# Kernel optimization log

Measured on AMD Instinct MI355X. Metric: run time of the kernel, lower is better.

The kernel has to match this reference:

```python
import jax, jax.numpy as jnp
import numpy as np

HIDDEN = 768
HEADS = 12
HEAD_DIM = HIDDEN // HEADS
NORM = float(np.sqrt(HIDDEN))  # module divides by sqrt(hidden_size), not sqrt(head_dim)


def setup_inputs() -> dict:
    key = jax.random.key(0)
    ks = jax.random.split(key, 7)
    B, S, H = 8, 1024, HIDDEN
    scale = 0.02
    return {
        "hidden_states": jax.random.normal(ks[0], (B, S, H), dtype=jnp.float32),
        "Wq": jax.random.normal(ks[1], (H, H), dtype=jnp.float32) * scale,
        "bq": jax.random.normal(ks[2], (H,), dtype=jnp.float32) * scale,
        "Wk": jax.random.normal(ks[3], (H, H), dtype=jnp.float32) * scale,
        "bk": jax.random.normal(ks[4], (H,), dtype=jnp.float32) * scale,
        "Wv": jax.random.normal(ks[5], (H, H), dtype=jnp.float32) * scale,
        "bv": jax.random.normal(ks[6], (H,), dtype=jnp.float32) * scale,
    }


def reference(hidden_states, Wq, bq, Wk, bk, Wv, bv):
    B, S, H = hidden_states.shape
    def heads(x):  # [B,S,H] -> [B,nh,S,hd]
        return x.reshape(B, S, HEADS, HEAD_DIM).transpose(0, 2, 1, 3)
    q = heads(hidden_states @ Wq + bq)
    k = heads(hidden_states @ Wk + bk)
    v = heads(hidden_states @ Wv + bv)
    # naive quadratic attention (world_size=1 ring): scores materialized
    scores = jnp.einsum("bhqd,bhkd->bhqk", q, k) / NORM
    probs = jax.nn.softmax(scores, axis=-1)  # dropout prob = 0.0
    ctx = jnp.einsum("bhqk,bhkd->bhqd", probs, v)
    # [B,nh,S,hd] -> [B,S,H]
    return ctx.transpose(0, 2, 1, 3).reshape(B, S, H)
```

## Files before the change

### kernel.cpp

```cpp
#include <hip/hip_runtime.h>
#include <hip/hip_bf16.h>
#include <stdint.h>

typedef __attribute__((ext_vector_type(8))) short short8;
typedef __attribute__((ext_vector_type(4))) float f32x4;
typedef __attribute__((ext_vector_type(4))) int i32x4;
typedef __attribute__((ext_vector_type(2))) int i32x2;
typedef __attribute__((ext_vector_type(4))) unsigned short u16x4;

#define HIDDEN 768
#define HEADS 12
#define HD 64
#define NB 8
#define SEQ 1024
#define MTOT (NB*SEQ)
#define QSCALE 0.05205887314427834f

typedef const __attribute__((address_space(1))) uint32_t* gas1_t;
typedef __attribute__((address_space(3))) uint32_t* las3_t;
#define GL_LDS16(g, l) __builtin_amdgcn_global_load_lds((gas1_t)(g), (las3_t)(l), 16, 0, 0)

static __device__ __forceinline__ unsigned short f2bf(float f){
  uint32_t u = __builtin_bit_cast(uint32_t, f);
  u += 0x7fffu + ((u >> 16) & 1u);
  return (unsigned short)(u >> 16);
}
static __device__ __forceinline__ float fexp2(float x){
#if __has_builtin(__builtin_amdgcn_exp2f)
  return __builtin_amdgcn_exp2f(x);
#else
  return exp2f(x);
#endif
}

__global__ void convert_x_kernel(const float* __restrict__ x, unsigned short* __restrict__ xb){
  int i = blockIdx.x * 256 + threadIdx.x;
  float4 v = reinterpret_cast<const float4*>(x)[i];
  u16x4 o;
  o[0]=f2bf(v.x); o[1]=f2bf(v.y); o[2]=f2bf(v.z); o[3]=f2bf(v.w);
  reinterpret_cast<u16x4*>(xb)[i] = o;
}

__global__ void transpose_w_kernel(const float* __restrict__ Wq, const float* __restrict__ Wk,
                                   const float* __restrict__ Wv, unsigned short* __restrict__ Wt){
  __shared__ float t[32][33];
  int z = blockIdx.z;
  const float* W = (z==0) ? Wq : ((z==1) ? Wk : Wv);
  unsigned short* o = Wt + (size_t)z * HIDDEN * HIDDEN;
  int n0 = blockIdx.x * 32, k0 = blockIdx.y * 32;
  int x = threadIdx.x & 31, y0 = threadIdx.x >> 5;
#pragma unroll
  for(int p=0;p<4;p++){ int y = y0 + p*8; t[y][x] = W[(size_t)(k0+y)*HIDDEN + n0 + x]; }
  __syncthreads();
#pragma unroll
  for(int p=0;p<4;p++){ int y = y0 + p*8; o[(size_t)(n0+y)*HIDDEN + k0 + x] = f2bf(t[x][y]); }
}

__global__ __launch_bounds__(256, 4) void gemm_qkv_kernel(
    const unsigned short* __restrict__ Xb, const unsigned short* __restrict__ Wt,
    const float* __restrict__ bq, const float* __restrict__ bk, const float* __restrict__ bv,
    unsigned short* __restrict__ Qg, unsigned short* __restrict__ Kg, unsigned short* __restrict__ Vt)
{
  __shared__ alignas(16) unsigned short lA[64*64];
  __shared__ alignas(16) unsigned short lB[128*64];
  int wgid = blockIdx.x;
  int xcd = wgid & 7, idx = wgid >> 3;
  int y = xcd + 8*(idx/18);
  int within = idx % 18;
  int xb = within % 6, z = within / 6;
  const unsigned short* W = Wt + (size_t)z*HIDDEN*HIDDEN;
  const float* bias = (z==0) ? bq : ((z==1) ? bk : bv);
  int m0 = y * 64, n0 = xb * 128;
  int tid = threadIdx.x;
  int w = tid >> 6, lane = tid & 63, l16 = lane & 15, g = lane >> 4;
  int wm = w >> 1, wn = w & 1;
  f32x4 acc[2][4] = {};
  for(int kt=0; kt<HIDDEN; kt+=64){
    __syncthreads();
#pragma unroll
    for(int p=0;p<2;p++){
      int t2 = p*256 + tid;
      int r = t2 >> 3;
      int cb = (((t2 & 7) << 4) ^ ((r & 7) << 4));
      GL_LDS16(Xb + (size_t)(m0 + r)*HIDDEN + kt + (cb >> 1), lA + p*2048 + w*512);
    }
#pragma unroll
    for(int p=0;p<4;p++){
      int t2 = p*256 + tid;
      int r = t2 >> 3;
      int cb = (((t2 & 7) << 4) ^ ((r & 7) << 4));
      GL_LDS16(W + (size_t)(n0 + r)*HIDDEN + kt + (cb >> 1), lB + p*2048 + w*512);
    }
    __syncthreads();
#pragma unroll
    for(int kk=0;kk<2;kk++){
      short8 af[2], bf[4];
#pragma unroll
      for(int i=0;i<2;i++){
        int row = wm*32 + i*16 + l16;
        af[i] = *reinterpret_cast<const short8*>(
            reinterpret_cast<const unsigned char*>(lA) + row*128 + ((kk*64 + g*16) ^ ((row&7)<<4)));
      }
#pragma unroll
      for(int j=0;j<4;j++){
        int row = wn*64 + j*16 + l16;
        bf[j] = *reinterpret_cast<const short8*>(
            reinterpret_cast<const unsigned char*>(lB) + row*128 + ((kk*64 + g*16) ^ ((row&7)<<4)));
      }
#pragma unroll
      for(int i=0;i<2;i++)
#pragma unroll
        for(int j=0;j<4;j++)
          acc[i][j] = __builtin_amdgcn_mfma_f32_16x16x32_bf16(af[i], bf[j], acc[i][j], 0, 0, 0);
    }
  }
  if(z == 2){
#pragma unroll
    for(int i=0;i<2;i++){
      int mb = m0 + wm*32 + i*16 + g*4;
      int b = mb >> 10, s = mb & 1023;
#pragma unroll
      for(int j=0;j<4;j++){
        int n = n0 + wn*64 + j*16 + l16;
        float bi = bias[n];
        int h = n >> 6, d = n & 63;
        u16x4 pk;
#pragma unroll
        for(int r=0;r<4;r++) pk[r] = f2bf(acc[i][j][r] + bi);
        *reinterpret_cast<u16x4*>(Vt + ((size_t)(b*HEADS + h)*HD + d)*SEQ + s) = pk;
      }
    }
  } else {
    unsigned short* out = (z==0) ? Qg : Kg;
#pragma unroll
    for(int i=0;i<2;i++){
      int mb = m0 + wm*32 + i*16 + g*4;
#pragma unroll
      for(int j=0;j<4;j++){
        int n = n0 + wn*64 + j*16 + l16;
        float bi = bias[n];
        int h = n >> 6, d = n & 63;
#pragma unroll
        for(int r=0;r<4;r++){
          int m = mb + r;
          int b = m >> 10, s = m & 1023;
          float cv = acc[i][j][r] + bi;
          if(z == 0) cv *= QSCALE;
          out[((size_t)(b*HEADS + h)*SEQ + s)*HD + d] = f2bf(cv);
        }
      }
    }
  }
}

__global__ __launch_bounds__(256, 3) void attn_kernel(
    const unsigned short* __restrict__ Qg, const unsigned short* __restrict__ Kg,
    const unsigned short* __restrict__ Vt, float* __restrict__ out)
{
  __shared__ alignas(16) unsigned short lK[2][64*64];
  __shared__ alignas(16) unsigned short lV[2][64*64];
  int wgid = blockIdx.x;
  int xcd = wgid & 7, ix = wgid >> 3;
  int bh = xcd*12 + (ix >> 3), qb = ix & 7;
  int b = bh / HEADS, h = bh % HEADS;
  int tid = threadIdx.x, w = tid >> 6, lane = tid & 63, l16 = lane & 15, g = lane >> 4;

  const unsigned short* Qbase = Qg + ((size_t)bh*SEQ + qb*128 + w*32)*HD;
  short8 qA0 = *reinterpret_cast<const short8*>(Qbase + l16*HD + g*8);
  short8 qA1 = *reinterpret_cast<const short8*>(Qbase + l16*HD + 32 + g*8);
  short8 qB0 = *reinterpret_cast<const short8*>(Qbase + (16+l16)*HD + g*8);
  short8 qB1 = *reinterpret_cast<const short8*>(Qbase + (16+l16)*HD + 32 + g*8);

  f32x4 oacc[2][4] = {};
  float lpart[2] = {0.f, 0.f};

  int sw = (l16 & 7) << 4;
  int ro0 = l16*128 + ((g*16) ^ sw);
  int ro1 = l16*128 + ((64 + g*16) ^ sw);
  int vo00 = l16*128 + ((      8*g) ^ sw);
  int vo01 = l16*128 + ((32  + 8*g) ^ sw);
  int vo10 = l16*128 + ((64  + 8*g) ^ sw);
  int vo11 = l16*128 + ((96  + 8*g) ^ sw);
  const unsigned char* lKb = reinterpret_cast<const unsigned char*>(&lK[0][0]);
  const unsigned char* lVb = reinterpret_cast<const unsigned char*>(&lV[0][0]);

  int r0 = tid >> 3;
  int cb0 = (((tid & 7) << 4) ^ ((r0 & 7) << 4)) >> 1;
  const unsigned short* gK0 = Kg + (size_t)bh*SEQ*HD + r0*HD + cb0;
  const unsigned short* gV0 = Vt + (size_t)bh*HD*SEQ + r0*SEQ + cb0;

#define STAGE(B, t) do { \
    GL_LDS16(gK0 + (t)*4096,          &lK[B][0] + w*512); \
    GL_LDS16(gK0 + (t)*4096 + 2048,   &lK[B][0] + 2048 + w*512); \
    GL_LDS16(gV0 + (t)*64,            &lV[B][0] + w*512); \
    GL_LDS16(gV0 + (t)*64 + 32*SEQ,   &lV[B][0] + 2048 + w*512); \
  } while(0)

#define SMPV(SREG, LP, OA) do { \
    int Wlo[4], Whi[4]; \
    _Pragma("unroll") for(int j=0;j<4;j++){ \
      float p0=fexp2(SREG[j][0]), p1=fexp2(SREG[j][1]); \
      float p2=fexp2(SREG[j][2]), p3=fexp2(SREG[j][3]); \
      LP += (p0+p1)+(p2+p3); \
      asm("v_cvt_pk_bf16_f32 %0, %1, %2" : "=v"(Wlo[j]) : "v"(p0), "v"(p1)); \
      asm("v_cvt_pk_bf16_f32 %0, %1, %2" : "=v"(Whi[j]) : "v"(p2), "v"(p3)); } \
    _Pragma("unroll") for(int m=0;m<2;m++){ \
      i32x4 cc; cc[0]=Wlo[2*m]; cc[1]=Whi[2*m]; cc[2]=Wlo[2*m+1]; cc[3]=Whi[2*m+1]; \
      short8 pB = __builtin_bit_cast(short8, cc); \
      _Pragma("unroll") for(int jn=0;jn<4;jn++) \
        OA[jn] = __builtin_amdgcn_mfma_f32_16x16x32_bf16(vf[jn][m], pB, OA[jn], 0,0,0); } \
  } while(0)

#define TILE(CUR, kt, HAS_NEXT) do { \
    if(HAS_NEXT) STAGE((CUR)^1, (kt)+1); \
    short8 kf[4][2]; \
    _Pragma("unroll") for(int j=0;j<4;j++){ \
      kf[j][0] = *reinterpret_cast<const short8*>(lKb + (CUR)*8192 + j*2048 + ro0); \
      kf[j][1] = *reinterpret_cast<const short8*>(lKb + (CUR)*8192 + j*2048 + ro1); } \
    short8 vf[4][2]; \
    _Pragma("unroll") for(int jn=0;jn<4;jn++){ \
      { i32x2 vl = *reinterpret_cast<const i32x2*>(lVb + (CUR)*8192 + jn*2048 + vo00); \
        i32x2 vh = *reinterpret_cast<const i32x2*>(lVb + (CUR)*8192 + jn*2048 + vo01); \
        i32x4 vc; vc[0]=vl[0]; vc[1]=vl[1]; vc[2]=vh[0]; vc[3]=vh[1]; \
        vf[jn][0] = __builtin_bit_cast(short8, vc); } \
      { i32x2 vl = *reinterpret_cast<const i32x2*>(lVb + (CUR)*8192 + jn*2048 + vo10); \
        i32x2 vh = *reinterpret_cast<const i32x2*>(lVb + (CUR)*8192 + jn*2048 + vo11); \
        i32x4 vc; vc[0]=vl[0]; vc[1]=vl[1]; vc[2]=vh[0]; vc[3]=vh[1]; \
        vf[jn][1] = __builtin_bit_cast(short8, vc); } } \
    f32x4 s0[4], s1[4]; \
    _Pragma("unroll") for(int j=0;j<4;j++){ \
      f32x4 zz = {}; \
      zz    = __builtin_amdgcn_mfma_f32_16x16x32_bf16(kf[j][0], qA0, zz, 0,0,0); \
      s0[j] = __builtin_amdgcn_mfma_f32_16x16x32_bf16(kf[j][1], qA1, zz, 0,0,0); } \
    _Pragma("unroll") for(int j=0;j<4;j++){ \
      f32x4 zz = {}; \
      zz    = __builtin_amdgcn_mfma_f32_16x16x32_bf16(kf[j][0], qB0, zz, 0,0,0); \
      s1[j] = __builtin_amdgcn_mfma_f32_16x16x32_bf16(kf[j][1], qB1, zz, 0,0,0); } \
    SMPV(s0, lpart[0], oacc[0]); \
    SMPV(s1, lpart[1], oacc[1]); \
    __syncthreads(); \
  } while(0)

  STAGE(0, 0);
  __syncthreads();

  for(int kt=0; kt<SEQ/64; kt+=2){
    TILE(0, kt, true);
    TILE(1, kt+1, (kt+1) < SEQ/64 - 1);
  }

#pragma unroll
  for(int rg=0;rg<2;rg++){
    float tot = lpart[rg];
    tot += __shfl_xor(tot, 16, 64);
    tot += __shfl_xor(tot, 32, 64);
    float invl = 1.0f / tot;
    int s = qb*128 + w*32 + rg*16 + l16;
    float* orow = out + ((size_t)b*SEQ + s)*HIDDEN + h*HD + 4*g;
#pragma unroll
    for(int jn=0;jn<4;jn++){
      float4 val;
      val.x = oacc[rg][jn][0]*invl; val.y = oacc[rg][jn][1]*invl;
      val.z = oacc[rg][jn][2]*invl; val.w = oacc[rg][jn][3]*invl;
      *reinterpret_cast<float4*>(orow + 16*jn) = val;
    }
  }
#undef STAGE
#undef SMPV
#undef TILE
}

extern "C" void kernel_launch(void* const* d_in, const int* in_sizes, int n_in,
                              void* d_out, int out_size, void* d_ws, size_t ws_size,
                              hipStream_t stream) {
  const float* hs = (const float*)d_in[0];
  const float* Wq = (const float*)d_in[1];
  const float* bq = (const float*)d_in[2];
  const float* Wk = (const float*)d_in[3];
  const float* bk = (const float*)d_in[4];
  const float* Wv = (const float*)d_in[5];
  const float* bv = (const float*)d_in[6];
  float* out = (float*)d_out;

  char* ws = (char*)d_ws;
  unsigned short* Xb = (unsigned short*)ws;
  unsigned short* Wt = (unsigned short*)(ws + (size_t)12582912);
  unsigned short* Qg = (unsigned short*)(ws + (size_t)16121856);
  unsigned short* Kg = Qg + (size_t)MTOT*HIDDEN;
  unsigned short* Vt = Kg + (size_t)MTOT*HIDDEN;

  convert_x_kernel<<<MTOT*HIDDEN/4/256, 256, 0, stream>>>(hs, Xb);
  transpose_w_kernel<<<dim3(24,24,3), 256, 0, stream>>>(Wq, Wk, Wv, Wt);
  gemm_qkv_kernel<<<2304, 256, 0, stream>>>(Xb, Wt, bq, bk, bv, Qg, Kg, Vt);
  attn_kernel<<<768, 256, 0, stream>>>(Qg, Kg, Vt, out);
}
```

Measured before the change: 90.48 us.

## Double-buffer LDS tiles in QKV GEMM to overlap loads with MFMA

The QKV projection GEMM now uses two LDS buffers for the A and B tiles. It issues the global-to-LDS loads for the next k-tile before computing on the current one, and needs one barrier per iteration instead of two. Global address arithmetic is also hoisted out of the loop. This is meant to hide global load latency behind MFMA work, at the cost of twice the LDS per block (48KB), which may limit occupancy to fewer than the 4 blocks the launch bounds request.

```diff
diff --git a/kernel.cpp b/kernel.cpp
--- a/kernel.cpp
+++ b/kernel.cpp
@@ -61,8 +61,8 @@
     const float* __restrict__ bq, const float* __restrict__ bk, const float* __restrict__ bv,
     unsigned short* __restrict__ Qg, unsigned short* __restrict__ Kg, unsigned short* __restrict__ Vt)
 {
-  __shared__ alignas(16) unsigned short lA[64*64];
-  __shared__ alignas(16) unsigned short lB[128*64];
+  __shared__ alignas(16) unsigned short lA[2][64*64];
+  __shared__ alignas(16) unsigned short lB[2][128*64];
   int wgid = blockIdx.x;
   int xcd = wgid & 7, idx = wgid >> 3;
   int y = xcd + 8*(idx/18);
@@ -74,46 +74,47 @@
   int tid = threadIdx.x;
   int w = tid >> 6, lane = tid & 63, l16 = lane & 15, g = lane >> 4;
   int wm = w >> 1, wn = w & 1;
+
+  int rs = tid >> 3;
+  int cbs = (((tid & 7) << 4) ^ ((rs & 7) << 4)) >> 1;
+  const unsigned short* gA0 = Xb + (size_t)(m0 + rs)*HIDDEN + cbs;
+  const unsigned short* gB0 = W  + (size_t)(n0 + rs)*HIDDEN + cbs;
+  const unsigned char* lAb = reinterpret_cast<const unsigned char*>(&lA[0][0]);
+  const unsigned char* lBb = reinterpret_cast<const unsigned char*>(&lB[0][0]);
+
   f32x4 acc[2][4] = {};
-  for(int kt=0; kt<HIDDEN; kt+=64){
+
+#define STAGE(BF, t) do { \
+    GL_LDS16(gA0 + (t)*64,                    &lA[BF][0] + w*512); \
+    GL_LDS16(gA0 + (size_t)32*HIDDEN + (t)*64, &lA[BF][0] + 2048 + w*512); \
+    _Pragma("unroll") for(int p=0;p<4;p++) \
+      GL_LDS16(gB0 + (size_t)p*32*HIDDEN + (t)*64, &lB[BF][0] + p*2048 + w*512); \
+  } while(0)
+
+#define COMPUTE(CUR) do { _Pragma("unroll") for(int kk=0;kk<2;kk++){ \
+    short8 af[2], bf[4]; \
+    _Pragma("unroll") for(int i=0;i<2;i++){ \
+      int row = wm*32 + i*16 + l16; \
+      af[i] = *reinterpret_cast<const short8*>( \
+          lAb + (CUR)*8192 + row*128 + ((kk*64 + g*16) ^ ((row&7)<<4))); } \
+    _Pragma("unroll") for(int j=0;j<4;j++){ \
+      int row = wn*64 + j*16 + l16; \
+      bf[j] = *reinterpret_cast<const short8*>( \
+          lBb + (CUR)*16384 + row*128 + ((kk*64 + g*16) ^ ((row&7)<<4))); } \
+    _Pragma("unroll") for(int i=0;i<2;i++) \
+      _Pragma("unroll") for(int j=0;j<4;j++) \
+        acc[i][j] = __builtin_amdgcn_mfma_f32_16x16x32_bf16(af[i], bf[j], acc[i][j], 0, 0, 0); \
+  } } while(0)
+
+  STAGE(0, 0);
+  __syncthreads();
+  for(int t=0; t<12; t++){
+    int cur = t & 1;
+    if(t < 11) STAGE(cur^1, t+1);
+    COMPUTE(cur);
     __syncthreads();
-#pragma unroll
-    for(int p=0;p<2;p++){
-      int t2 = p*256 + tid;
-      int r = t2 >> 3;
-      int cb = (((t2 & 7) << 4) ^ ((r & 7) << 4));
-      GL_LDS16(Xb + (size_t)(m0 + r)*HIDDEN + kt + (cb >> 1), lA + p*2048 + w*512);
-    }
-#pragma unroll
-    for(int p=0;p<4;p++){
-      int t2 = p*256 + tid;
-      int r = t2 >> 3;
-      int cb = (((t2 & 7) << 4) ^ ((r & 7) << 4));
-      GL_LDS16(W + (size_t)(n0 + r)*HIDDEN + kt + (cb >> 1), lB + p*2048 + w*512);
-    }
-    __syncthreads();
-#pragma unroll
-    for(int kk=0;kk<2;kk++){
-      short8 af[2], bf[4];
-#pragma unroll
-      for(int i=0;i<2;i++){
-        int row = wm*32 + i*16 + l16;
-        af[i] = *reinterpret_cast<const short8*>(
-            reinterpret_cast<const unsigned char*>(lA) + row*128 + ((kk*64 + g*16) ^ ((row&7)<<4)));
-      }
-#pragma unroll
-      for(int j=0;j<4;j++){
-        int row = wn*64 + j*16 + l16;
-        bf[j] = *reinterpret_cast<const short8*>(
-            reinterpret_cast<const unsigned char*>(lB) + row*128 + ((kk*64 + g*16) ^ ((row&7)<<4)));
-      }
-#pragma unroll
-      for(int i=0;i<2;i++)
-#pragma unroll
-        for(int j=0;j<4;j++)
-          acc[i][j] = __builtin_amdgcn_mfma_f32_16x16x32_bf16(af[i], bf[j], acc[i][j], 0, 0, 0);
-    }
-  }
+  }
+
   if(z == 2){
 #pragma unroll
     for(int i=0;i<2;i++){
@@ -151,6 +152,8 @@
       }
     }
   }
+#undef STAGE
+#undef COMPUTE
 }
 
 __global__ __launch_bounds__(256, 3) void attn_kernel(
```

Measured after the change: 96.14 us. 6.3% more time.
